# Optimization experiments

Measured on AMD Instinct MI355X. Metric: run time of the kernel, lower is better.

Reference implementation:

```python
import jax, jax.numpy as jnp
import numpy as np

EPS = 1e-8
CG_TOL = 1e-4
S_SIGMA = 8   # bilateral grid spatial downsampling
N_BINS = 9    # bilateral grid range bins (intensity in [0,1])


def _conv2d(x, k):
    # x [C,H,W], k [kh,kw] -> same-padded cross-correlation, per channel
    kh, kw = k.shape
    out = jax.lax.conv_general_dilated(x[:, None], k[None, None], (1, 1),
                                       [(kh // 2, kh // 2), (kw // 2, kw // 2)])
    return out[:, 0]


def _conv2d_T(x, k):
    return _conv2d(x, k[::-1, ::-1])


def _conv_bank(x, ks):
    # x [C,H,W], ks [N,kh,kw] -> [N,C,H,W]
    n, kh, kw = ks.shape
    out = jax.lax.conv_general_dilated(x[:, None], ks[:, None], (1, 1),
                                       [(kh // 2, kh // 2), (kw // 2, kw // 2)])
    return out.transpose(1, 0, 2, 3)


def _conv_bank_T(v, ks):
    # v [N,C,H,W] -> sum_n conv(v[n], flip(ks[n])) : [C,H,W]
    n, kh, kw = ks.shape
    lhs = v.transpose(1, 0, 2, 3)          # [C,N,H,W]
    rhs = ks[:, ::-1, ::-1][None]          # [1,N,kh,kw]
    out = jax.lax.conv_general_dilated(lhs, rhs, (1, 1),
                                       [(kh // 2, kh // 2), (kw // 2, kw // 2)])
    return out[:, 0]


def _deconv_grad(blurred, x, kernel, dkw, dks, rkw, rks, rpow, reg_targets):
    # gradient of E(x) = sum_i dkw_i ||dk_i * (k*x - b)||^2
    #                  + sum_j rkw_j sum |rk_j*x - t_j|^{p_j}
    Kx = _conv2d(x, kernel) - blurred
    d = _conv_bank(Kx, dks)                                    # [Nd,C,H,W]
    g = _conv2d_T(_conv_bank_T(2.0 * dkw[:, None, None, None] * d, dks), kernel)
    v = _conv_bank(x, rks) - reg_targets                       # [Nr,C,H,W]
    av = jnp.abs(v) + EPS
    phi = jnp.sign(v) * av ** (rpow[:, None, None, None] - 1.0)
    g = g + _conv_bank_T(rkw[:, None, None, None] * rpow[:, None, None, None] * phi, rks)
    return g


def _deconv_alpha(blurred, x, kernel, dkw, dks, rkw, rks, rpow, reg_targets, p):
    # exact line search for the quadratic part, Gauss-Newton for |.|^p prior
    g = _deconv_grad(blurred, x, kernel, dkw, dks, rkw, rks, rpow, reg_targets)
    num = -jnp.sum(g * p)
    Kp = _conv2d(p, kernel)
    dKp = _conv_bank(Kp, dks)
    den = jnp.sum(2.0 * dkw[:, None, None, None] * dKp ** 2)
    v = _conv_bank(x, rks) - reg_targets
    Rp = _conv_bank(p, rks)
    w = (rkw * rpow * (rpow - 1.0))[:, None, None, None]
    den = den + jnp.sum(w * (jnp.abs(v) + EPS) ** (rpow[:, None, None, None] - 2.0) * Rp ** 2)
    return num / (den + 1e-12)


def _deconv_prior(x, rks, thr):
    # soft-shrinkage of filtered responses -> regularization targets
    v = _conv_bank(x, rks)
    return jnp.sign(v) * jnp.maximum(jnp.abs(v) - thr[:, None, None, None], 0.0)


def _conv_axis(g, f, axis):
    k = f.shape[0]; r = k // 2; L = g.shape[axis]
    pad = [(0, 0)] * g.ndim; pad[axis] = (r, r)
    gp = jnp.pad(g, pad)
    out = jnp.zeros_like(g)
    for t in range(k):  # fixed small tap count
        out = out + f[t] * jax.lax.slice_in_dim(gp, t, t + L, axis=axis)
    return out


def _bilateral_channel(I, fs, fr):
    # learned-filter bilateral grid: splat -> separable filter (fs,fs,fr) -> trilinear slice
    H, W = I.shape
    gh, gw = H // S_SIGMA, W // S_SIGMA
    Ic = jnp.clip(I, 0.0, 1.0)
    yy, xx = jnp.meshgrid(jnp.arange(H), jnp.arange(W), indexing="ij")
    yi = yy // S_SIGMA; xi = xx // S_SIGMA
    zi = jnp.clip(jnp.round(Ic * (N_BINS - 1)).astype(jnp.int32), 0, N_BINS - 1)
    flat = ((yi * gw + xi) * N_BINS + zi).ravel()
    gv = jnp.zeros(gh * gw * N_BINS, Ic.dtype).at[flat].add(Ic.ravel())
    gw_ = jnp.zeros(gh * gw * N_BINS, Ic.dtype).at[flat].add(1.0)
    g2 = jnp.stack([gv, gw_], -1).reshape(gh, gw, N_BINS, 2)
    g2 = _conv_axis(_conv_axis(_conv_axis(g2, fs, 0), fs, 1), fr, 2)
    yf = yy / S_SIGMA; xf = xx / S_SIGMA; zf = Ic * (N_BINS - 1)

    def corners(f, n):
        c0 = jnp.clip(jnp.floor(f).astype(jnp.int32), 0, n - 1)
        c1 = jnp.minimum(c0 + 1, n - 1)
        w = jnp.clip(f - c0, 0.0, 1.0)
        return c0, c1, w

    y0, y1, wy = corners(yf, gh)
    x0, x1, wx = corners(xf, gw)
    z0, z1, wz = corners(zf, N_BINS)
    acc = jnp.zeros(I.shape + (2,), Ic.dtype)
    for yc, wyc in ((y0, 1 - wy), (y1, wy)):
        for xc, wxc in ((x0, 1 - wx), (x1, wx)):
            for zc, wzc in ((z0, 1 - wz), (z1, wz)):
                acc = acc + (wyc * wxc * wzc)[..., None] * g2[yc, xc, zc]
    return acc[..., 0] / (acc[..., 1] + 1e-8)


def _forward(blurred_batch, kernel_batch, data_kernels, data_kernel_weights,
             reg_kernels, reg_kernel_weights, reg_powers, filter_s, filter_r,
             reg_thresholds, num_cg_iter):
    num_stages = filter_s.shape[0]
    n_reg = reg_kernels.shape[1]

    def single(blurred, kernel):
        def cg(x, idx, reg_targets):
            dkw = data_kernel_weights[idx]; dks = data_kernels[idx]
            rkw = reg_kernel_weights[idx]; rks = reg_kernels[idx]; rp = reg_powers[idx]
            g = _deconv_grad(blurred, x, kernel, dkw, dks, rkw, rks, rp, reg_targets)
            r = -g
            r_norm = jnp.sum(r * r)
            r0 = r_norm

            def body(i, carry):
                x, r, p, rn, done = carry
                alpha = _deconv_alpha(blurred, x, kernel, dkw, dks, rkw, rks, rp, reg_targets, p)
                x1 = x + alpha * p
                g1 = _deconv_grad(blurred, x1, kernel, dkw, dks, rkw, rks, rp, reg_targets)
                r1 = -g1
                nrn = jnp.sum(r1 * r1)
                beta = nrn / (rn + 1e-20)
                conv_now = nrn < CG_TOL * r0
                p1 = r1 + beta * p
                x_n = jnp.where(done, x, x1)
                r_n = jnp.where(done, r, r1)
                rn_n = jnp.where(done, rn, nrn)
                p_n = jnp.where(done | conv_now, p, p1)
                return (x_n, r_n, p_n, rn_n, done | conv_now)

            carry = (x, r, r, r_norm, jnp.array(False))
            x, _, _, _, _ = jax.lax.fori_loop(0, num_cg_iter, body, carry)
            return x

        x = cg(blurred, 0, jnp.zeros((n_reg,) + blurred.shape, blurred.dtype))
        for stage in range(num_stages):
            x = jax.vmap(lambda ch: _bilateral_channel(ch, filter_s[stage], filter_r[stage]))(x)
            reg_targets = _deconv_prior(x, reg_kernels[stage + 1], reg_thresholds[stage])
            x = cg(x, stage + 1, reg_targets)
        return x

    return jax.vmap(single)(blurred_batch, kernel_batch)


def setup_inputs() -> dict:
    key = jax.random.key(0)
    k1, k2 = jax.random.split(key)
    B, C, H, W, KS = 2, 3, 512, 512, 15
    blurred = jax.random.uniform(k1, (B, C, H, W), jnp.float32)
    kern = jax.random.uniform(k2, (B, KS, KS), jnp.float32)
    kern = kern / jnp.sum(kern, axis=(1, 2), keepdims=True)  # normalized PSFs

    ns = 1; c = 2  # num_stages, kernel center (5x5)
    rk = np.zeros((ns + 1, 5, 5, 5), np.float32)
    rk[:, 0, c, c] = -1.0; rk[:, 0, c + 1, c] = 1.0
    rk[:, 1, c, c] = -1.0; rk[:, 1, c, c + 1] = 1.0
    rk[:, 2, c, c] = 1.0; rk[:, 2, c + 1, c] = -1.0
    rk[:, 2, c, c + 1] = -1.0; rk[:, 2, c + 1, c + 1] = 1.0
    rk[:, 3, c - 1, c] = 1.0; rk[:, 3, c, c] = -2.0; rk[:, 3, c + 1, c] = 1.0
    rk[:, 4, c, c - 1] = 1.0; rk[:, 4, c, c] = -2.0; rk[:, 4, c, c + 1] = 1.0
    dk = np.zeros((ns + 1, 6, 5, 5), np.float32)
    dk[:, 0, c, c] = 1.0
    dk[:, 1:] = rk
    dkw = np.zeros((ns + 1, 6), np.float32); dkw[:, 0] = 1.0
    rkw = np.zeros((ns + 1, 5), np.float32)
    rkw[0, :] = 0.001; rkw[1:, :] = 0.05
    rpow = np.full((ns + 1, 5), 2.0, np.float32)
    fs = np.zeros((ns, 11), np.float32); fs[:, 3:8] = [0.0, 1.0, 2.0, 1.0, 0.0]
    fr = np.tile(np.array([0.0, 1.0, 2.0, 1.0, 0.0], np.float32), (ns, 1))
    thr = np.tile(np.array([0.065, 0.065, 0.0325, 0.0325, 0.0325], np.float32), (ns, 1))

    return {
        "blurred_batch": blurred,
        "kernel_batch": kern,
        "data_kernels": jnp.asarray(dk),
        "data_kernel_weights": jnp.asarray(dkw),
        "reg_kernels": jnp.asarray(rk),
        "reg_kernel_weights": jnp.asarray(rkw),
        "reg_powers": jnp.asarray(rpow),
        "filter_s": jnp.asarray(fs),
        "filter_r": jnp.asarray(fr),
        "reg_thresholds": jnp.asarray(thr),
        "num_cg_iter": 5,
    }


def reference(blurred_batch, kernel_batch, data_kernels, data_kernel_weights,
              reg_kernels, reg_kernel_weights, reg_powers, filter_s, filter_r,
              reg_thresholds, num_cg_iter):
    return _forward(blurred_batch, kernel_batch, data_kernels, data_kernel_weights,
                    reg_kernels, reg_kernel_weights, reg_powers, filter_s, filter_r,
                    reg_thresholds, num_cg_iter)
```

## Files before the change

### kernel.cpp

```cpp
#include <hip/hip_runtime.h>

constexpr int Bn = 2, Cn = 3, Hh = 512, Ww = 512;
constexpr int KS = 15, KR = 7;
constexpr int NDK = 6, NRK = 5;
constexpr int GH = 64, GW = 64, NBn = 9, SS = 8;
constexpr float EPSf = 1e-8f;
constexpr float CGTOL = 1e-4f;
constexpr int PLANE = Hh * Ww;
constexpr int CHW = Cn * PLANE;
constexpr int BX = 64, BY = 16;
constexpr int GXc = Ww / BX, GYc = Hh / BY;
constexpr int PB = GXc * GYc * Cn;
constexpr int SA = 80, THt = 30;
constexpr int S2W = 72, S2H = 24;
constexpr int PHW = 68, PHH = 20;
constexpr int PHG = (PHW / 4) * PHH;
constexpr int NITER = 5;

struct CgState { float alpha, beta, rn, r0; int done, pflag; int pad0, pad1; };

struct SolveInfo {
    int fastBank;
    int allrp2;
    int nd;
    int pad;
    float sctot;
    float dsc[NDK];
    int ddy[NDK], ddx[NDK];
    float C[81];
};

__device__ __forceinline__ float blockReduce(float v, float* red, int tid) {
    red[tid] = v; __syncthreads();
    for (int s = 128; s > 0; s >>= 1) { if (tid < s) red[tid] += red[tid + s]; __syncthreads(); }
    float r = red[0]; __syncthreads();
    return r;
}

__global__ __launch_bounds__(128)
void k_comp(const float* __restrict__ dkw, const float* __restrict__ dks,
            const float* __restrict__ rkw, const float* __restrict__ rpw,
            const float* __restrict__ rks, SolveInfo* si)
{
    const int idx = blockIdx.x;
    SolveInfo* s = si + idx;
    const float* dkw_i = dkw + idx * NDK;
    const float* dks_i = dks + (size_t)idx * NDK * 25;
    const float* rkw_i = rkw + idx * NRK;
    const float* rpw_i = rpw + idx * NRK;
    const float* rks_i = rks + (size_t)idx * NRK * 25;
    const int t = threadIdx.x;
    if (t < 81) {
        int oy = t / 9 - 4, ox = t % 9 - 4;
        float acc = 0.f;
        for (int m = 0; m < NRK; m++) {
            float wm = rkw_i[m], rp = rpw_i[m];
            float ch = wm * rp * (rp - 1.f);
            if (ch == 0.f) continue;
            for (int ay = 0; ay < 5; ay++)
                for (int ax = 0; ax < 5; ax++) {
                    int by = ay - oy, bx = ax - ox;
                    if (by < 0 || by >= 5 || bx < 0 || bx >= 5) continue;
                    acc += ch * rks_i[m * 25 + ay * 5 + ax] * rks_i[m * 25 + by * 5 + bx];
                }
        }
        s->C[t] = acc;
    }
    if (t == 81) {
        int fast = 1, nd = 0; float tot = 0.f;
        for (int n = 0; n < NDK; n++) {
            if (dkw_i[n] == 0.f) continue;
            int cnt = 0, pos = -1;
            for (int q = 0; q < 25; q++) if (dks_i[n * 25 + q] != 0.f) { cnt++; pos = q; }
            if (cnt > 1) fast = 0;
            if (cnt == 1 && nd < NDK) {
                float v = dks_i[n * 25 + pos];
                s->dsc[nd] = 2.f * dkw_i[n] * v * v;
                s->ddy[nd] = pos / 5 - 2; s->ddx[nd] = pos % 5 - 2;
                tot += s->dsc[nd]; nd++;
            }
        }
        s->fastBank = fast; s->nd = fast ? nd : 0; s->sctot = tot;
    }
    if (t == 82) {
        int ok = 1;
        for (int m = 0; m < NRK; m++) {
            float wm = rkw_i[m], rp = rpw_i[m];
            if (wm != 0.f && rp != 2.f && wm * rp * (rp - 1.f) != 0.f) ok = 0;
        }
        s->allrp2 = ok;
    }
}

__global__ __launch_bounds__(256)
void k_conv15(const float* __restrict__ src, const float* __restrict__ rb,
              const float* __restrict__ pbuf, float* __restrict__ aux2,
              const float* __restrict__ sub, float* __restrict__ out,
              const float* __restrict__ kernB, float* __restrict__ part,
              const SolveInfo* __restrict__ si,
              const CgState* __restrict__ st, const int* __restrict__ ncg,
              int iter, int mode)
{
    const int pz = blockIdx.z, b = pz / Cn, c = pz % Cn;
    const CgState s = st[b];
    if (mode == 2 && (s.done != 0 || iter >= *ncg)) return;
    __shared__ __align__(16) float tile[SA * THt];
    __shared__ float red[256];
    const int tx = threadIdx.x, ty = threadIdx.y, tid = ty * 16 + tx;
    const int ox0 = blockIdx.x * BX, oy0 = blockIdx.y * BY;
    const int baseP = pz * PLANE;
    const float beta = s.beta; const int pf = s.pflag;
    const float* kp = kernB + b * 225;

    float nm = 0.f;
    for (int i = tid; i < 78 * THt; i += 256) {
        int ly = i / 78, lx = i % 78;
        int gy = oy0 - KR + ly, gx = ox0 - KR + lx;
        float v = 0.f;
        if (gy >= 0 && gy < Hh && gx >= 0 && gx < Ww) {
            int gi = baseP + gy * Ww + gx;
            if (mode == 2) {
                float rv = rb[gi], pv = pbuf[gi];
                v = pf ? fmaf(beta, pv, rv) : pv;
                if (ly >= KR && ly < KR + BY && lx >= KR && lx < KR + BX) {
                    nm = fmaf(rv, v, nm);
                    aux2[gi] = v;
                }
            } else {
                v = src[gi];
                if (mode == 0 && ly >= KR && ly < KR + BY && lx >= KR && lx < KR + BX)
                    aux2[gi] = v;
            }
        }
        tile[ly * SA + lx] = v;
    }
    __syncthreads();

    const int colbase = tx * 4;
    float a0 = 0.f, a1 = 0.f, a2 = 0.f, a3 = 0.f;
    for (int i = 0; i < KS; i++) {
        const float4* rp4 = reinterpret_cast<const float4*>(&tile[(ty + i) * SA + colbase]);
        float f[20];
        #pragma unroll
        for (int s5 = 0; s5 < 5; s5++) {
            float4 w4 = rp4[s5];
            f[s5 * 4] = w4.x; f[s5 * 4 + 1] = w4.y; f[s5 * 4 + 2] = w4.z; f[s5 * 4 + 3] = w4.w;
        }
        const float* kr = kp + i * 15;
        #pragma unroll
        for (int j = 0; j < KS; j++) {
            float kv = kr[j];
            a0 = fmaf(kv, f[j], a0); a1 = fmaf(kv, f[j + 1], a1);
            a2 = fmaf(kv, f[j + 2], a2); a3 = fmaf(kv, f[j + 3], a3);
        }
    }
    const int gi = baseP + (oy0 + ty) * Ww + ox0 + colbase;
    if (sub) {
        float4 sv = *reinterpret_cast<const float4*>(&sub[gi]);
        a0 -= sv.x; a1 -= sv.y; a2 -= sv.z; a3 -= sv.w;
    }
    if (si->fastBank) {
        const int gy = oy0 + ty, gx0 = ox0 + colbase;
        if (gy >= 2 && gy <= Hh - 3 && gx0 >= 2 && gx0 + 3 <= Ww - 3) {
            float sc = si->sctot;
            a0 *= sc; a1 *= sc; a2 *= sc; a3 *= sc;
        } else {
            float m0 = 0.f, m1 = 0.f, m2 = 0.f, m3 = 0.f;
            int ndl = si->nd;
            for (int n = 0; n < ndl; n++) {
                float sc = si->dsc[n]; int dy = si->ddy[n], dx = si->ddx[n];
                if (gy - dy < 0 || gy - dy >= Hh) continue;
                if (gx0     - dx >= 0 && gx0     - dx < Ww) m0 += sc;
                if (gx0 + 1 - dx >= 0 && gx0 + 1 - dx < Ww) m1 += sc;
                if (gx0 + 2 - dx >= 0 && gx0 + 2 - dx < Ww) m2 += sc;
                if (gx0 + 3 - dx >= 0 && gx0 + 3 - dx < Ww) m3 += sc;
            }
            a0 *= m0; a1 *= m1; a2 *= m2; a3 *= m3;
        }
    }
    *reinterpret_cast<float4*>(&out[gi]) = make_float4(a0, a1, a2, a3);
    if (mode == 2) {
        float tot = blockReduce(nm, red, tid);
        if (tid == 0) {
            int blk = c * (GXc * GYc) + blockIdx.y * GXc + blockIdx.x;
            part[((size_t)b * 4 + 0) * PB + blk] = tot;
        }
    }
}

__global__ __launch_bounds__(256)
void k_bank(const float* __restrict__ sbuf, float* __restrict__ tbuf,
            const float* __restrict__ dks, const float* __restrict__ dkw,
            const SolveInfo* __restrict__ si,
            const CgState* __restrict__ st, const int* __restrict__ ncg,
            int iter, int mode)
{
    if (si->fastBank) return;
    const int pz = blockIdx.z, b = pz / Cn;
    if (mode == 1 && (st[b].done != 0 || iter >= *ncg)) return;
    __shared__ __align__(16) float sl[S2W * S2H];
    __shared__ __align__(16) float dl[PHW * PHH];
    __shared__ float dkk[NDK * 25];
    __shared__ float dww[NDK];
    const int tx = threadIdx.x, ty = threadIdx.y, tid = ty * 16 + tx;
    const int ox0 = blockIdx.x * BX, oy0 = blockIdx.y * BY;
    const int baseP = pz * PLANE;
    const int colbase = tx * 4;
    for (int i = tid; i < NDK * 25; i += 256) dkk[i] = dks[i];
    if (tid < NDK) dww[tid] = dkw[tid];
    for (int i = tid; i < S2W * S2H; i += 256) {
        int ly = i / S2W, lx = i % S2W;
        int gy = oy0 - 4 + ly, gx = ox0 - 4 + lx;
        sl[i] = (gy >= 0 && gy < Hh && gx >= 0 && gx < Ww) ? sbuf[baseP + gy * Ww + gx] : 0.f;
    }
    __syncthreads();
    float t0 = 0.f, t1 = 0.f, t2 = 0.f, t3 = 0.f;
    for (int n = 0; n < NDK; n++) {
        float wn = 2.f * dww[n];
        if (wn == 0.f) continue;
        float dnr[25];
        #pragma unroll
        for (int q = 0; q < 25; q++) dnr[q] = dkk[n * 25 + q];
        for (int t = tid; t < PHG; t += 256) {
            int zy = t / 17, zx0 = (t % 17) * 4;
            int gy = oy0 - 2 + zy, gx0 = ox0 - 2 + zx0;
            float v0 = 0.f, v1 = 0.f, v2 = 0.f, v3 = 0.f;
            #pragma unroll
            for (int a = 0; a < 5; a++) {
                bool rz = dnr[a*5]==0.f && dnr[a*5+1]==0.f && dnr[a*5+2]==0.f &&
                          dnr[a*5+3]==0.f && dnr[a*5+4]==0.f;
                if (rz) continue;
                const float4* s4 = reinterpret_cast<const float4*>(&sl[(zy + a) * S2W + zx0]);
                float4 u0 = s4[0], u1 = s4[1];
                float f8[8] = {u0.x,u0.y,u0.z,u0.w,u1.x,u1.y,u1.z,u1.w};
                #pragma unroll
                for (int bb = 0; bb < 5; bb++) {
                    float kv = dnr[a * 5 + bb];
                    if (kv != 0.f) {
                        v0 = fmaf(kv, f8[bb], v0); v1 = fmaf(kv, f8[bb+1], v1);
                        v2 = fmaf(kv, f8[bb+2], v2); v3 = fmaf(kv, f8[bb+3], v3);
                    }
                }
            }
            bool gyin = (gy >= 0 && gy < Hh);
            if (!gyin || gx0     < 0 || gx0     >= Ww) v0 = 0.f;
            if (!gyin || gx0 + 1 < 0 || gx0 + 1 >= Ww) v1 = 0.f;
            if (!gyin || gx0 + 2 < 0 || gx0 + 2 >= Ww) v2 = 0.f;
            if (!gyin || gx0 + 3 < 0 || gx0 + 3 >= Ww) v3 = 0.f;
            *reinterpret_cast<float4*>(&dl[zy * PHW + zx0]) = make_float4(v0, v1, v2, v3);
        }
        __syncthreads();
        float c0 = 0.f, c1 = 0.f, c2 = 0.f, c3 = 0.f;
        #pragma unroll
        for (int a = 0; a < 5; a++) {
            int fr = 4 - a;
            bool rz = dnr[fr*5]==0.f && dnr[fr*5+1]==0.f && dnr[fr*5+2]==0.f &&
                      dnr[fr*5+3]==0.f && dnr[fr*5+4]==0.f;
            if (rz) continue;
            const float4* q4 = reinterpret_cast<const float4*>(&dl[(ty + a) * PHW + colbase]);
            float4 u0 = q4[0], u1 = q4[1];
            float f8[8] = {u0.x,u0.y,u0.z,u0.w,u1.x,u1.y,u1.z,u1.w};
            #pragma unroll
            for (int bb = 0; bb < 5; bb++) {
                float kv = dnr[fr * 5 + (4 - bb)];
                if (kv != 0.f) {
                    c0 = fmaf(kv, f8[bb], c0); c1 = fmaf(kv, f8[bb+1], c1);
                    c2 = fmaf(kv, f8[bb+2], c2); c3 = fmaf(kv, f8[bb+3], c3);
                }
            }
        }
        t0 = fmaf(wn, c0, t0); t1 = fmaf(wn, c1, t1);
        t2 = fmaf(wn, c2, t2); t3 = fmaf(wn, c3, t3);
        __syncthreads();
    }
    const int gi = baseP + (oy0 + ty) * Ww + ox0 + colbase;
    *reinterpret_cast<float4*>(&tbuf[gi]) = make_float4(t0, t1, t2, t3);
}

__global__ __launch_bounds__(256)
void k_hess(const float* __restrict__ kx, const float* __restrict__ wb,
            const float* __restrict__ pn,
            float* __restrict__ qb, const float* __restrict__ kernB,
            const float* __restrict__ rks, const float* __restrict__ rkw,
            const float* __restrict__ rpw, const SolveInfo* __restrict__ si,
            float* __restrict__ part, const CgState* __restrict__ st,
            const int* __restrict__ ncg, int iter)
{
    if (!si->allrp2) return;
    const int pz = blockIdx.z, b = pz / Cn, c = pz % Cn;
    const CgState s = st[b];
    if (s.done != 0 || iter >= *ncg) return;
    __shared__ __align__(16) float wt[SA * THt];
    __shared__ __align__(16) float s2[S2W * S2H];
    __shared__ __align__(16) float sC[81];
    __shared__ float rk5[NRK * 25];
    __shared__ float srkw[NRK], srpw[NRK];
    __shared__ float red[256];
    float* ph = wt;
    const int tx = threadIdx.x, ty = threadIdx.y, tid = ty * 16 + tx;
    const int ox0 = blockIdx.x * BX, oy0 = blockIdx.y * BY;
    const int baseP = pz * PLANE;
    const float* wsrc = si->fastBank ? kx : wb;
    const float* kp = kernB + b * 225;

    for (int i = tid; i < 81; i += 256) sC[i] = si->C[i];
    for (int i = tid; i < NRK * 25; i += 256) rk5[i] = rks[i];
    if (tid < NRK) { srkw[tid] = rkw[tid]; srpw[tid] = rpw[tid]; }

    for (int i = tid; i < 78 * THt; i += 256) {
        int ly = i / 78, lx = i % 78;
        int gy = oy0 - KR + ly, gx = ox0 - KR + lx;
        wt[ly * SA + lx] = (gy >= 0 && gy < Hh && gx >= 0 && gx < Ww)
                           ? wsrc[baseP + gy * Ww + gx] : 0.f;
    }
    for (int i = tid; i < S2W * S2H; i += 256) {
        int ly = i / S2W, lx = i % S2W;
        int gy = oy0 - 4 + ly, gx = ox0 - 4 + lx;
        s2[i] = (gy >= 0 && gy < Hh && gx >= 0 && gx < Ww)
                ? pn[baseP + gy * Ww + gx] : 0.f;
    }
    __syncthreads();

    const int colbase = tx * 4;
    float a0 = 0.f, a1 = 0.f, a2 = 0.f, a3 = 0.f;
    for (int i = 0; i < KS; i++) {
        const float4* rp4 = reinterpret_cast<const float4*>(&wt[(ty + i) * SA + colbase]);
        float f[20];
        #pragma unroll
        for (int s5 = 0; s5 < 5; s5++) {
            float4 w4 = rp4[s5];
            f[s5 * 4] = w4.x; f[s5 * 4 + 1] = w4.y; f[s5 * 4 + 2] = w4.z; f[s5 * 4 + 3] = w4.w;
        }
        const float* kr = kp + (14 - i) * 15;
        #pragma unroll
        for (int j = 0; j < KS; j++) {
            float kv = kr[14 - j];
            a0 = fmaf(kv, f[j], a0); a1 = fmaf(kv, f[j + 1], a1);
            a2 = fmaf(kv, f[j + 2], a2); a3 = fmaf(kv, f[j + 3], a3);
        }
    }

    const bool blkInterior = (oy0 >= 2) && (oy0 + BY - 1 <= Hh - 3) &&
                             (ox0 >= 2) && (ox0 + BX - 1 <= Ww - 3);
    if (blkInterior) {
        #pragma unroll
        for (int oy = 0; oy < 9; oy++) {
            float cr[9]; bool nz = false;
            #pragma unroll
            for (int ox = 0; ox < 9; ox++) { cr[ox] = sC[oy * 9 + ox]; nz = nz || (cr[ox] != 0.f); }
            if (!nz) continue;
            const float4* s4 = reinterpret_cast<const float4*>(&s2[(ty + oy) * S2W + colbase]);
            float4 u0 = s4[0], u1 = s4[1], u2 = s4[2];
            float f12[12] = {u0.x,u0.y,u0.z,u0.w,u1.x,u1.y,u1.z,u1.w,u2.x,u2.y,u2.z,u2.w};
            #pragma unroll
            for (int ox = 0; ox < 9; ox++) {
                float kv = cr[ox];
                if (kv != 0.f) {
                    a0 = fmaf(kv, f12[ox], a0); a1 = fmaf(kv, f12[ox + 1], a1);
                    a2 = fmaf(kv, f12[ox + 2], a2); a3 = fmaf(kv, f12[ox + 3], a3);
                }
            }
        }
    } else {
        __syncthreads();
        for (int m = 0; m < NRK; m++) {
            float wm = srkw[m], rp = srpw[m];
            float coefH = wm * rp * (rp - 1.f);
            if (coefH == 0.f) continue;
            float rmr[25];
            #pragma unroll
            for (int q = 0; q < 25; q++) rmr[q] = rk5[m * 25 + q];
            for (int t = tid; t < PHG; t += 256) {
                int zy = t / 17, zx0 = (t % 17) * 4;
                int gy = oy0 - 2 + zy, gx0 = ox0 - 2 + zx0;
                float v0 = 0.f, v1 = 0.f, v2 = 0.f, v3 = 0.f;
                #pragma unroll
                for (int a = 0; a < 5; a++) {
                    bool rz = rmr[a*5]==0.f && rmr[a*5+1]==0.f && rmr[a*5+2]==0.f &&
                              rmr[a*5+3]==0.f && rmr[a*5+4]==0.f;
                    if (rz) continue;
                    const float4* s4 = reinterpret_cast<const float4*>(&s2[(zy + a) * S2W + zx0]);
                    float4 u0 = s4[0], u1 = s4[1];
                    float f8[8] = {u0.x,u0.y,u0.z,u0.w,u1.x,u1.y,u1.z,u1.w};
                    #pragma unroll
                    for (int bb = 0; bb < 5; bb++) {
                        float kv = rmr[a * 5 + bb];
                        if (kv != 0.f) {
                            v0 = fmaf(kv, f8[bb], v0); v1 = fmaf(kv, f8[bb+1], v1);
                            v2 = fmaf(kv, f8[bb+2], v2); v3 = fmaf(kv, f8[bb+3], v3);
                        }
                    }
                }
                bool gyin = (gy >= 0 && gy < Hh);
                if (!gyin || gx0     < 0 || gx0     >= Ww) v0 = 0.f;
                if (!gyin || gx0 + 1 < 0 || gx0 + 1 >= Ww) v1 = 0.f;
                if (!gyin || gx0 + 2 < 0 || gx0 + 2 >= Ww) v2 = 0.f;
                if (!gyin || gx0 + 3 < 0 || gx0 + 3 >= Ww) v3 = 0.f;
                *reinterpret_cast<float4*>(&ph[zy * PHW + zx0]) =
                    make_float4(coefH * v0, coefH * v1, coefH * v2, coefH * v3);
            }
            __syncthreads();
            #pragma unroll
            for (int a = 0; a < 5; a++) {
                int fr = 4 - a;
                bool rz = rmr[fr*5]==0.f && rmr[fr*5+1]==0.f && rmr[fr*5+2]==0.f &&
                          rmr[fr*5+3]==0.f && rmr[fr*5+4]==0.f;
                if (rz) continue;
                const float4* q4 = reinterpret_cast<const float4*>(&ph[(ty + a) * PHW + colbase]);
                float4 u0 = q4[0], u1 = q4[1];
                float f8[8] = {u0.x,u0.y,u0.z,u0.w,u1.x,u1.y,u1.z,u1.w};
                #pragma unroll
                for (int bb = 0; bb < 5; bb++) {
                    float kv = rmr[fr * 5 + (4 - bb)];
                    if (kv != 0.f) {
                        a0 = fmaf(kv, f8[bb], a0); a1 = fmaf(kv, f8[bb+1], a1);
                        a2 = fmaf(kv, f8[bb+2], a2); a3 = fmaf(kv, f8[bb+3], a3);
                    }
                }
            }
            __syncthreads();
        }
    }

    const int gy = oy0 + ty, gx0 = ox0 + colbase;
    const int gi = baseP + gy * Ww + gx0;
    *reinterpret_cast<float4*>(&qb[gi]) = make_float4(a0, a1, a2, a3);
    int li = (ty + 4) * S2W + colbase + 4;
    float redv = s2[li] * a0 + s2[li + 1] * a1 + s2[li + 2] * a2 + s2[li + 3] * a3;
    float tot = blockReduce(redv, red, tid);
    if (tid == 0) {
        int blk = c * (GXc * GYc) + blockIdx.y * GXc + blockIdx.x;
        part[((size_t)b * 4 + 1) * PB + blk] = tot;
    }
}

__global__ __launch_bounds__(256)
void k_gradL(const float* __restrict__ kx, const float* __restrict__ wb,
             const float* __restrict__ xg,
             const float* __restrict__ rb, const float* __restrict__ pbuf,
             const float* __restrict__ tgt, const float* __restrict__ thr,
             float* __restrict__ outb,
             float* __restrict__ pout, const float* __restrict__ kernB,
             const float* __restrict__ rks, const float* __restrict__ rkw,
             const float* __restrict__ rpw, const SolveInfo* __restrict__ si,
             float* __restrict__ part, const CgState* __restrict__ st,
             const int* __restrict__ ncg, int iter, int mode)
{
    if (mode == 1 && si->allrp2) return;
    const int pz = blockIdx.z, b = pz / Cn, c = pz % Cn;
    const CgState s = st[b];
    if (mode == 1 && (s.done != 0 || iter >= *ncg)) return;
    __shared__ __align__(16) float wt[SA * THt];
    __shared__ __align__(16) float s2[S2W * S2H];
    __shared__ __align__(16) float sC[81];
    __shared__ float rk5[NRK * 25];
    __shared__ float srkw[NRK], srpw[NRK], sthr[NRK];
    __shared__ float red[256];
    float* ph = wt;
    const int tx = threadIdx.x, ty = threadIdx.y, tid = ty * 16 + tx;
    const int ox0 = blockIdx.x * BX, oy0 = blockIdx.y * BY;
    const int baseP = pz * PLANE;
    const float beta = s.beta; const int pf = s.pflag;
    const float* wsrc = si->fastBank ? kx : wb;
    const float* kp = kernB + b * 225;

    for (int i = tid; i < 81; i += 256) sC[i] = si->C[i];
    for (int i = tid; i < NRK * 25; i += 256) rk5[i] = rks[i];
    if (tid < NRK) {
        srkw[tid] = rkw[tid]; srpw[tid] = rpw[tid];
        sthr[tid] = thr ? thr[tid] : 0.f;
    }

    for (int i = tid; i < 78 * THt; i += 256) {
        int ly = i / 78, lx = i % 78;
        int gy = oy0 - KR + ly, gx = ox0 - KR + lx;
        wt[ly * SA + lx] = (gy >= 0 && gy < Hh && gx >= 0 && gx < Ww)
                           ? wsrc[baseP + gy * Ww + gx] : 0.f;
    }
    for (int i = tid; i < S2W * S2H; i += 256) {
        int ly = i / S2W, lx = i % S2W;
        int gy = oy0 - 4 + ly, gx = ox0 - 4 + lx;
        float v = 0.f;
        if (gy >= 0 && gy < Hh && gx >= 0 && gx < Ww) {
            int gi = baseP + gy * Ww + gx;
            if (mode == 0) v = xg[gi];
            else { float rv = rb[gi], pv = pbuf[gi]; v = pf ? fmaf(beta, pv, rv) : pv; }
        }
        s2[i] = v;
    }
    __syncthreads();

    const int colbase = tx * 4;
    float a0 = 0.f, a1 = 0.f, a2 = 0.f, a3 = 0.f;
    for (int i = 0; i < KS; i++) {
        const float4* rp4 = reinterpret_cast<const float4*>(&wt[(ty + i) * SA + colbase]);
        float f[20];
        #pragma unroll
        for (int s5 = 0; s5 < 5; s5++) {
            float4 w4 = rp4[s5];
            f[s5 * 4] = w4.x; f[s5 * 4 + 1] = w4.y; f[s5 * 4 + 2] = w4.z; f[s5 * 4 + 3] = w4.w;
        }
        const float* kr = kp + (14 - i) * 15;
        #pragma unroll
        for (int j = 0; j < KS; j++) {
            float kv = kr[14 - j];
            a0 = fmaf(kv, f[j], a0); a1 = fmaf(kv, f[j + 1], a1);
            a2 = fmaf(kv, f[j + 2], a2); a3 = fmaf(kv, f[j + 3], a3);
        }
    }

    const bool blkInterior = (oy0 >= 2) && (oy0 + BY - 1 <= Hh - 3) &&
                             (ox0 >= 2) && (ox0 + BX - 1 <= Ww - 3);
    if (mode == 0 && si->allrp2 && thr == nullptr && blkInterior) {
        #pragma unroll
        for (int oy = 0; oy < 9; oy++) {
            float cr[9]; bool nz = false;
            #pragma unroll
            for (int ox = 0; ox < 9; ox++) { cr[ox] = sC[oy * 9 + ox]; nz = nz || (cr[ox] != 0.f); }
            if (!nz) continue;
            const float4* s4 = reinterpret_cast<const float4*>(&s2[(ty + oy) * S2W + colbase]);
            float4 u0 = s4[0], u1 = s4[1], u2 = s4[2];
            float f12[12] = {u0.x,u0.y,u0.z,u0.w,u1.x,u1.y,u1.z,u1.w,u2.x,u2.y,u2.z,u2.w};
            #pragma unroll
            for (int ox = 0; ox < 9; ox++) {
                float kv = cr[ox];
                if (kv != 0.f) {
                    a0 = fmaf(kv, f12[ox], a0); a1 = fmaf(kv, f12[ox + 1], a1);
                    a2 = fmaf(kv, f12[ox + 2], a2); a3 = fmaf(kv, f12[ox + 3], a3);
                }
            }
        }
    } else {
        __syncthreads();
        for (int m = 0; m < NRK; m++) {
            float wm = srkw[m], rp = srpw[m];
            if (wm == 0.f) continue;
            float rmr[25];
            #pragma unroll
            for (int q = 0; q < 25; q++) rmr[q] = rk5[m * 25 + q];
            const float* tgm = (mode == 1 && tgt)
                ? tgt + ((size_t)(b * NRK + m)) * CHW + (size_t)c * PLANE : nullptr;
            const float coefG = wm * rp;
            const float coefH = wm * rp * (rp - 1.f);
            const float thrm = sthr[m];

            for (int t = tid; t < PHG; t += 256) {
                int zy = t / 17, zx0 = (t % 17) * 4;
                int gy = oy0 - 2 + zy, gx0 = ox0 - 2 + zx0;
                float v0 = 0.f, v1 = 0.f, v2 = 0.f, v3 = 0.f;
                #pragma unroll
                for (int a = 0; a < 5; a++) {
                    bool rz = rmr[a*5]==0.f && rmr[a*5+1]==0.f && rmr[a*5+2]==0.f &&
                              rmr[a*5+3]==0.f && rmr[a*5+4]==0.f;
                    if (rz) continue;
                    const float4* s4 = reinterpret_cast<const float4*>(&s2[(zy + a) * S2W + zx0]);
                    float4 u0 = s4[0], u1 = s4[1];
                    float f8[8] = {u0.x,u0.y,u0.z,u0.w,u1.x,u1.y,u1.z,u1.w};
                    #pragma unroll
                    for (int bb = 0; bb < 5; bb++) {
                        float kv = rmr[a * 5 + bb];
                        if (kv != 0.f) {
                            v0 = fmaf(kv, f8[bb], v0); v1 = fmaf(kv, f8[bb+1], v1);
                            v2 = fmaf(kv, f8[bb+2], v2); v3 = fmaf(kv, f8[bb+3], v3);
                        }
                    }
                }
                bool gyin = (gy >= 0 && gy < Hh);
                float o0 = 0.f, o1 = 0.f, o2 = 0.f, o3 = 0.f;
                #pragma unroll
                for (int j = 0; j < 4; j++) {
                    int gx = gx0 + j;
                    if (!gyin || gx < 0 || gx >= Ww) continue;
                    float v = (j == 0) ? v0 : (j == 1) ? v1 : (j == 2) ? v2 : v3;
                    float o;
                    if (mode == 0) {
                        if (thr) {
                            float sgv = (v > 0.f) ? 1.f : ((v < 0.f) ? -1.f : 0.f);
                            v = sgv * fminf(fabsf(v), thrm);
                        }
                        float sg = (v > 0.f) ? 1.f : ((v < 0.f) ? -1.f : 0.f);
                        float av = fabsf(v) + EPSf;
                        o = coefG * sg * ((rp == 2.f) ? av : powf(av, rp - 1.f));
                    } else {
                        float fac = 1.f;
                        if (rp != 2.f) {
                            float vx = 0.f;
                            for (int a = 0; a < 5; a++)
                                for (int bb = 0; bb < 5; bb++) {
                                    int yy = gy - 2 + a, xx = gx - 2 + bb;
                                    if (yy >= 0 && yy < Hh && xx >= 0 && xx < Ww)
                                        vx = fmaf(rmr[a * 5 + bb], xg[baseP + yy * Ww + xx], vx);
                                }
                            if (tgm) vx -= tgm[gy * Ww + gx];
                            fac = powf(fabsf(vx) + EPSf, rp - 2.f);
                        }
                        o = coefH * fac * v;
                    }
                    if (j == 0) o0 = o; else if (j == 1) o1 = o; else if (j == 2) o2 = o; else o3 = o;
                }
                *reinterpret_cast<float4*>(&ph[zy * PHW + zx0]) = make_float4(o0, o1, o2, o3);
            }
            __syncthreads();
            #pragma unroll
            for (int a = 0; a < 5; a++) {
                int fr = 4 - a;
                bool rz = rmr[fr*5]==0.f && rmr[fr*5+1]==0.f && rmr[fr*5+2]==0.f &&
                          rmr[fr*5+3]==0.f && rmr[fr*5+4]==0.f;
                if (rz) continue;
                const float4* q4 = reinterpret_cast<const float4*>(&ph[(ty + a) * PHW + colbase]);
                float4 u0 = q4[0], u1 = q4[1];
                float f8[8] = {u0.x,u0.y,u0.z,u0.w,u1.x,u1.y,u1.z,u1.w};
                #pragma unroll
                for (int bb = 0; bb < 5; bb++) {
                    float kv = rmr[fr * 5 + (4 - bb)];
                    if (kv != 0.f) {
                        a0 = fmaf(kv, f8[bb], a0); a1 = fmaf(kv, f8[bb+1], a1);
                        a2 = fmaf(kv, f8[bb+2], a2); a3 = fmaf(kv, f8[bb+3], a3);
                    }
                }
            }
            __syncthreads();
        }
    }

    const int gi = baseP + (oy0 + ty) * Ww + ox0 + colbase;
    float redv;
    if (mode == 0) {
        float r0v = -a0, r1v = -a1, r2v = -a2, r3v = -a3;
        float4 rv4 = make_float4(r0v, r1v, r2v, r3v);
        *reinterpret_cast<float4*>(&outb[gi]) = rv4;
        *reinterpret_cast<float4*>(&pout[gi]) = rv4;
        redv = r0v * r0v + r1v * r1v + r2v * r2v + r3v * r3v;
    } else {
        *reinterpret_cast<float4*>(&outb[gi]) = make_float4(a0, a1, a2, a3);
        int li = (ty + 4) * S2W + colbase + 4;
        redv = s2[li] * a0 + s2[li + 1] * a1 + s2[li + 2] * a2 + s2[li + 3] * a3;
    }
    float tot = blockReduce(redv, red, tid);
    if (tid == 0) {
        int blk = c * (GXc * GYc) + blockIdx.y * GXc + blockIdx.x;
        int slot = (mode == 0) ? 2 : 1;
        part[((size_t)b * 4 + slot) * PB + blk] = tot;
    }
}

__global__ __launch_bounds__(256)
void k_axpy(float4* __restrict__ x, float4* __restrict__ r,
            const float4* __restrict__ pn,
            const float4* __restrict__ q, float* __restrict__ part,
            const CgState* __restrict__ st, const int* __restrict__ ncg, int iter)
{
    const int b = blockIdx.y;
    const CgState s = st[b];
    if (s.done != 0 || iter >= *ncg) return;
    __shared__ float red[256];
    const int tid = threadIdx.x;
    const int idx = b * (CHW / 4) + blockIdx.x * 256 + tid;
    float4 pc = pn[idx], rv = r[idx], qv = q[idx], xv = x[idx];
    xv.x = fmaf(s.alpha, pc.x, xv.x); xv.y = fmaf(s.alpha, pc.y, xv.y);
    xv.z = fmaf(s.alpha, pc.z, xv.z); xv.w = fmaf(s.alpha, pc.w, xv.w);
    rv.x = fmaf(-s.alpha, qv.x, rv.x); rv.y = fmaf(-s.alpha, qv.y, rv.y);
    rv.z = fmaf(-s.alpha, qv.z, rv.z); rv.w = fmaf(-s.alpha, qv.w, rv.w);
    x[idx] = xv; r[idx] = rv;
    float nr = rv.x * rv.x + rv.y * rv.y + rv.z * rv.z + rv.w * rv.w;
    float tot = blockReduce(nr, red, tid);
    if (tid == 0) part[((size_t)b * 4 + 2) * PB + blockIdx.x] = tot;
}

__global__ __launch_bounds__(256)
void k_fin_alpha(const float* __restrict__ part, CgState* st,
                 const int* __restrict__ ncg, int iter)
{
    const int b = blockIdx.x, tid = threadIdx.x;
    __shared__ float red[256];
    if (st[b].done != 0 || iter >= *ncg) { if (tid == 0) st[b].alpha = 0.f; return; }
    float sn = 0.f, sd = 0.f;
    for (int i = tid; i < PB; i += 256) {
        sn += part[((size_t)b * 4 + 0) * PB + i];
        sd += part[((size_t)b * 4 + 1) * PB + i];
    }
    float num = blockReduce(sn, red, tid);
    float den = blockReduce(sd, red, tid);
    if (tid == 0) st[b].alpha = num / (den + 1e-12f);
}

__global__ __launch_bounds__(256)
void k_fin_iter(const float* __restrict__ part, CgState* st,
                const int* __restrict__ ncg, int iter, int mode)
{
    const int b = blockIdx.x, tid = threadIdx.x;
    __shared__ float red[256];
    if (mode == 1 && (st[b].done != 0 || iter >= *ncg)) { if (tid == 0) st[b].pflag = 0; return; }
    float s = 0.f;
    for (int i = tid; i < PB; i += 256) s += part[((size_t)b * 4 + 2) * PB + i];
    float nrn = blockReduce(s, red, tid);
    if (tid == 0) {
        if (mode == 0) {
            st[b].rn = nrn; st[b].r0 = nrn; st[b].done = 0; st[b].pflag = 0;
            st[b].beta = 0.f; st[b].alpha = 0.f;
        } else {
            float beta = nrn / (st[b].rn + 1e-20f);
            int conv = (nrn < CGTOL * st[b].r0) ? 1 : 0;
            st[b].beta = beta; st[b].rn = nrn;
            st[b].pflag = conv ? 0 : 1;
            if (conv) st[b].done = 1;
        }
    }
}

__global__ __launch_bounds__(64)
void k_splat(const float* __restrict__ x, float* __restrict__ grid)
{
    __shared__ float bins[NBn * 2];
    const int tid = threadIdx.y * 8 + threadIdx.x;
    if (tid < NBn * 2) bins[tid] = 0.f;
    __syncthreads();
    const int pz = blockIdx.z;
    const int gy = blockIdx.y, gx = blockIdx.x;
    const int py = gy * 8 + threadIdx.y, px = gx * 8 + threadIdx.x;
    float I = x[(size_t)pz * PLANE + py * Ww + px];
    float Ic = fminf(fmaxf(I, 0.f), 1.f);
    int zi = (int)rintf(Ic * (NBn - 1));
    zi = min(max(zi, 0), NBn - 1);
    atomicAdd(&bins[zi * 2], Ic);
    atomicAdd(&bins[zi * 2 + 1], 1.f);
    __syncthreads();
    if (tid < NBn * 2)
        grid[(size_t)pz * GH * GW * NBn * 2 + ((size_t)gy * GW + gx) * NBn * 2 + tid] = bins[tid];
}

__global__ __launch_bounds__(256)
void k_blur(const float* __restrict__ in, float* __restrict__ out,
            const float* __restrict__ taps, int ntaps, int axis)
{
    const int id = blockIdx.x * 256 + threadIdx.x;
    const int total = Bn * Cn * GH * GW * NBn;
    if (id >= total) return;
    const int z = id % NBn;
    const int x = (id / NBn) % GW;
    const int y = (id / (NBn * GW)) % GH;
    const int p = id / (NBn * GW * GH);
    int coord, lim; long stride;
    if (axis == 0)      { coord = y; lim = GH;  stride = (long)GW * NBn * 2; }
    else if (axis == 1) { coord = x; lim = GW;  stride = NBn * 2; }
    else                { coord = z; lim = NBn; stride = 2; }
    const long base = (((long)(p * GH + y) * GW + x) * NBn + z) * 2;
    const int r = ntaps / 2;
    float a0 = 0.f, a1 = 0.f;
    for (int t = 0; t < ntaps; t++) {
        int cc = coord + t - r;
        if (cc < 0 || cc >= lim) continue;
        float w = taps[t];
        long ofs = base + (long)(cc - coord) * stride;
        a0 = fmaf(w, in[ofs], a0);
        a1 = fmaf(w, in[ofs + 1], a1);
    }
    out[base] = a0; out[base + 1] = a1;
}

__global__ __launch_bounds__(256)
void k_slice(const float* __restrict__ xin, const float* __restrict__ grid,
             float* __restrict__ xout)
{
    const int pz = blockIdx.z;
    const int id = blockIdx.x * 256 + threadIdx.x;
    const int py = id / Ww, px = id % Ww;
    float I = xin[(size_t)pz * PLANE + id];
    float Ic = fminf(fmaxf(I, 0.f), 1.f);
    float yf = (float)py / SS, xf = (float)px / SS, zf = Ic * (NBn - 1);
    int y0 = min(max((int)floorf(yf), 0), GH - 1); int y1 = min(y0 + 1, GH - 1);
    float wy = fminf(fmaxf(yf - (float)y0, 0.f), 1.f);
    int x0 = min(max((int)floorf(xf), 0), GW - 1); int x1 = min(x0 + 1, GW - 1);
    float wx = fminf(fmaxf(xf - (float)x0, 0.f), 1.f);
    int z0 = min(max((int)floorf(zf), 0), NBn - 1); int z1 = min(z0 + 1, NBn - 1);
    float wz = fminf(fmaxf(zf - (float)z0, 0.f), 1.f);
    const float* gp = grid + (size_t)pz * GH * GW * NBn * 2;
    const int   ys[2] = { y0, y1 };  const float wys[2] = { 1.f - wy, wy };
    const int   xs[2] = { x0, x1 };  const float wxs[2] = { 1.f - wx, wx };
    const int   zs[2] = { z0, z1 };  const float wzs[2] = { 1.f - wz, wz };
    float a0 = 0.f, a1 = 0.f;
    for (int iy = 0; iy < 2; iy++)
        for (int ix = 0; ix < 2; ix++)
            for (int iz = 0; iz < 2; iz++) {
                float w = wys[iy] * wxs[ix] * wzs[iz];
                size_t idx = (((size_t)ys[iy] * GW + xs[ix]) * NBn + zs[iz]) * 2;
                a0 = fmaf(w, gp[idx], a0);
                a1 = fmaf(w, gp[idx + 1], a1);
            }
    xout[(size_t)pz * PLANE + id] = a0 / (a1 + 1e-8f);
}

__global__ __launch_bounds__(256)
void k_prior(const float* __restrict__ x, float* __restrict__ tgt,
             const float* __restrict__ rks, const float* __restrict__ thr,
             const SolveInfo* __restrict__ si)
{
    if (si->allrp2) return;
    const int pz = blockIdx.z, b = pz / Cn, c = pz % Cn;
    __shared__ float xl[24 * 24];
    __shared__ float rkk[NRK * 25];
    __shared__ float sthr[NRK];
    const int tx = threadIdx.x, ty = threadIdx.y, tid = ty * 16 + tx;
    const int ox0 = blockIdx.x * 16, oy0 = blockIdx.y * 16;
    const int baseP = pz * PLANE;
    for (int i = tid; i < NRK * 25; i += 256) rkk[i] = rks[i];
    if (tid < NRK) sthr[tid] = thr[tid];
    for (int i = tid; i < 24 * 24; i += 256) {
        int ly = i / 24, lx = i % 24;
        int gy = oy0 - 2 + ly, gx = ox0 - 2 + lx;
        xl[i] = (gy >= 0 && gy < Hh && gx >= 0 && gx < Ww) ? x[baseP + gy * Ww + gx] : 0.f;
    }
    __syncthreads();
    const int pix = (oy0 + ty) * Ww + (ox0 + tx);
    for (int m = 0; m < NRK; m++) {
        const float* rm = &rkk[m * 25];
        float v = 0.f;
        #pragma unroll
        for (int a = 0; a < 5; a++)
            #pragma unroll
            for (int bb = 0; bb < 5; bb++)
                v = fmaf(rm[a * 5 + bb], xl[(ty + a) * 24 + (tx + bb)], v);
        float sg = (v > 0.f) ? 1.f : ((v < 0.f) ? -1.f : 0.f);
        tgt[((size_t)(b * NRK + m)) * CHW + (size_t)c * PLANE + pix] =
            sg * fmaxf(fabsf(v) - sthr[m], 0.f);
    }
}

extern "C" void kernel_launch(void* const* d_in, const int* in_sizes, int n_in,
                              void* d_out, int out_size, void* d_ws, size_t ws_size,
                              hipStream_t stream)
{
    const float* blurred = (const float*)d_in[0];
    const float* kern    = (const float*)d_in[1];
    const float* dks     = (const float*)d_in[2];
    const float* dkw     = (const float*)d_in[3];
    const float* rks     = (const float*)d_in[4];
    const float* rkw     = (const float*)d_in[5];
    const float* rpw     = (const float*)d_in[6];
    const float* fs      = (const float*)d_in[7];
    const float* fr      = (const float*)d_in[8];
    const float* thr     = (const float*)d_in[9];
    const int*   ncg     = (const int*)d_in[10];
    (void)in_sizes; (void)n_in; (void)out_size; (void)ws_size;

    float* w = (float*)d_ws;
    size_t off = 0;
    auto alloc = [&](size_t n) { float* p = w + off; off += n; return p; };
    float* xb    = alloc((size_t)Bn * CHW);
    float* pbufA = alloc((size_t)Bn * CHW);
    float* pbufB = alloc((size_t)Bn * CHW);
    float* rbuf  = alloc((size_t)Bn * CHW);
    float* kx    = alloc((size_t)Bn * CHW);
    float* wb    = alloc((size_t)Bn * CHW);
    float* qb    = alloc((size_t)Bn * CHW);
    float* tg    = alloc((size_t)Bn * NRK * CHW);
    float* g0    = alloc((size_t)Bn * Cn * GH * GW * NBn * 2);
    float* g1    = alloc((size_t)Bn * Cn * GH * GW * NBn * 2);
    float* part  = alloc((size_t)Bn * 4 * PB);
    CgState* st = (CgState*)(w + off); off += Bn * 8;
    SolveInfo* sinf = (SolveInfo*)(w + off); off += 2 * ((sizeof(SolveInfo) + 3) / 4);

    dim3 tb(16, 16), grd(GXc, GYc, Bn * Cn);

    k_comp<<<2, 128, 0, stream>>>(dkw, dks, rkw, rpw, rks, sinf);

    auto solve = [&](int idx, const float* tgt, const float* thr_i, int initmode) {
        const float* dks_i = dks + (size_t)idx * NDK * 25;
        const float* dkw_i = dkw + (size_t)idx * NDK;
        const float* rks_i = rks + (size_t)idx * NRK * 25;
        const float* rkw_i = rkw + (size_t)idx * NRK;
        const float* rpw_i = rpw + (size_t)idx * NRK;
        const SolveInfo* si = sinf + idx;
        k_conv15<<<grd, tb, 0, stream>>>(initmode == 0 ? blurred : xb, nullptr, nullptr,
                                         initmode == 0 ? xb : nullptr, blurred, kx, kern,
                                         nullptr, si, st, ncg, 0, initmode == 0 ? 0 : 3);
        k_bank<<<grd, tb, 0, stream>>>(kx, wb, dks_i, dkw_i, si, st, ncg, 0, 0);
        k_gradL<<<grd, tb, 0, stream>>>(kx, wb, xb, nullptr, nullptr, tgt, thr_i,
                                        rbuf, pbufA, kern,
                                        rks_i, rkw_i, rpw_i, si, part, st, ncg, 0, 0);
        k_fin_iter<<<Bn, 256, 0, stream>>>(part, st, ncg, 0, 0);
        float* pcur = pbufA;
        float* pnxt = pbufB;
        for (int i = 0; i < NITER; i++) {
            k_conv15<<<grd, tb, 0, stream>>>(nullptr, rbuf, pcur, pnxt, nullptr, kx, kern,
                                             part, si, st, ncg, i, 2);
            k_bank<<<grd, tb, 0, stream>>>(kx, wb, dks_i, dkw_i, si, st, ncg, i, 1);
            k_hess<<<grd, tb, 0, stream>>>(kx, wb, pnxt, qb, kern,
                                           rks_i, rkw_i, rpw_i, si, part, st, ncg, i);
            k_gradL<<<grd, tb, 0, stream>>>(kx, wb, xb, rbuf, pnxt, tgt, thr_i, qb, nullptr, kern,
                                            rks_i, rkw_i, rpw_i, si, part, st, ncg, i, 1);
            k_fin_alpha<<<Bn, 256, 0, stream>>>(part, st, ncg, i);
            k_axpy<<<dim3(PB, Bn), 256, 0, stream>>>((float4*)xb, (float4*)rbuf,
                                                     (const float4*)pnxt,
                                                     (const float4*)qb, part, st, ncg, i);
            k_fin_iter<<<Bn, 256, 0, stream>>>(part, st, ncg, i, 1);
            float* tswap = pcur; pcur = pnxt; pnxt = tswap;
        }
    };

    solve(0, nullptr, nullptr, 0);

    dim3 sb(8, 8), sg(GW, GH, Bn * Cn);
    k_splat<<<sg, sb, 0, stream>>>(xb, g0);
    const int totalg = Bn * Cn * GH * GW * NBn;
    k_blur<<<(totalg + 255) / 256, 256, 0, stream>>>(g0, g1, fs, 11, 0);
    k_blur<<<(totalg + 255) / 256, 256, 0, stream>>>(g1, g0, fs, 11, 1);
    k_blur<<<(totalg + 255) / 256, 256, 0, stream>>>(g0, g1, fr, 5, 2);
    k_slice<<<dim3(PLANE / 256, 1, Bn * Cn), 256, 0, stream>>>(xb, g1, xb);

    k_prior<<<dim3(Ww / 16, Hh / 16, Bn * Cn), tb, 0, stream>>>(xb, tg, rks + NRK * 25, thr,
                                                                sinf + 1);

    solve(1, tg, thr, 1);

    hipMemcpyAsync(d_out, xb, (size_t)Bn * CHW * sizeof(float),
                   hipMemcpyDeviceToDevice, stream);
}
```

Measured before the change: 1.337 ms.

## Fold CG alpha and residual-norm reductions into axpy kernel

Each axpy block now recomputes alpha from the partial sums itself, so the separate k_fin_alpha launch is gone. A last-block-done atomic counter lets the final axpy block do the residual-norm reduction and the beta/convergence update, so k_fin_iter is also dropped inside the loop. This removes two small serial launches per CG iteration. In exchange every block redundantly reads the PB partials, and correctness now relies on atomics and threadfences.

```diff
diff --git a/kernel.cpp b/kernel.cpp
--- a/kernel.cpp
+++ b/kernel.cpp
@@ -37,10 +37,25 @@
     return r;
 }
 
+__device__ __forceinline__ bool lastBlockDone(unsigned int* c, unsigned int nb,
+                                              int tid, int* sflag) {
+    __syncthreads();
+    if (tid == 0) {
+        __threadfence();
+        unsigned int old = atomicAdd(c, 1u);
+        *sflag = (old == nb - 1u) ? 1 : 0;
+    }
+    __syncthreads();
+    bool last = (*sflag != 0);
+    if (last && tid == 0) __threadfence();
+    if (last) __syncthreads();
+    return last;
+}
+
 __global__ __launch_bounds__(128)
 void k_comp(const float* __restrict__ dkw, const float* __restrict__ dks,
             const float* __restrict__ rkw, const float* __restrict__ rpw,
-            const float* __restrict__ rks, SolveInfo* si)
+            const float* __restrict__ rks, SolveInfo* si, unsigned int* cnt)
 {
     const int idx = blockIdx.x;
     SolveInfo* s = si + idx;
@@ -50,6 +65,7 @@
     const float* rpw_i = rpw + idx * NRK;
     const float* rks_i = rks + (size_t)idx * NRK * 25;
     const int t = threadIdx.x;
+    if (idx == 0 && t < 8) cnt[t] = 0u;
     if (t < 81) {
         int oy = t / 9 - 4, ox = t % 9 - 4;
         float acc = 0.f;
@@ -70,10 +86,10 @@
         int fast = 1, nd = 0; float tot = 0.f;
         for (int n = 0; n < NDK; n++) {
             if (dkw_i[n] == 0.f) continue;
-            int cnt = 0, pos = -1;
-            for (int q = 0; q < 25; q++) if (dks_i[n * 25 + q] != 0.f) { cnt++; pos = q; }
-            if (cnt > 1) fast = 0;
-            if (cnt == 1 && nd < NDK) {
+            int cntz = 0, pos = -1;
+            for (int q = 0; q < 25; q++) if (dks_i[n * 25 + q] != 0.f) { cntz++; pos = q; }
+            if (cntz > 1) fast = 0;
+            if (cntz == 1 && nd < NDK) {
                 float v = dks_i[n * 25 + pos];
                 s->dsc[nd] = 2.f * dkw_i[n] * v * v;
                 s->ddy[nd] = pos / 5 - 2; s->ddx[nd] = pos % 5 - 2;
@@ -646,42 +662,47 @@
 
 __global__ __launch_bounds__(256)
 void k_axpy(float4* __restrict__ x, float4* __restrict__ r,
-            const float4* __restrict__ pn,
-            const float4* __restrict__ q, float* __restrict__ part,
-            const CgState* __restrict__ st, const int* __restrict__ ncg, int iter)
+            const float4* __restrict__ pn, const float4* __restrict__ q,
+            float* __restrict__ part, CgState* st,
+            const int* __restrict__ ncg, int iter, unsigned int* cnt)
 {
     const int b = blockIdx.y;
     const CgState s = st[b];
     if (s.done != 0 || iter >= *ncg) return;
     __shared__ float red[256];
+    __shared__ int sflag;
     const int tid = threadIdx.x;
+    float sn = 0.f, sd = 0.f;
+    for (int i = tid; i < PB; i += 256) {
+        sn += part[((size_t)b * 4 + 0) * PB + i];
+        sd += part[((size_t)b * 4 + 1) * PB + i];
+    }
+    float num = blockReduce(sn, red, tid);
+    float den = blockReduce(sd, red, tid);
+    const float alpha = num / (den + 1e-12f);
     const int idx = b * (CHW / 4) + blockIdx.x * 256 + tid;
     float4 pc = pn[idx], rv = r[idx], qv = q[idx], xv = x[idx];
-    xv.x = fmaf(s.alpha, pc.x, xv.x); xv.y = fmaf(s.alpha, pc.y, xv.y);
-    xv.z = fmaf(s.alpha, pc.z, xv.z); xv.w = fmaf(s.alpha, pc.w, xv.w);
-    rv.x = fmaf(-s.alpha, qv.x, rv.x); rv.y = fmaf(-s.alpha, qv.y, rv.y);
-    rv.z = fmaf(-s.alpha, qv.z, rv.z); rv.w = fmaf(-s.alpha, qv.w, rv.w);
+    xv.x = fmaf(alpha, pc.x, xv.x); xv.y = fmaf(alpha, pc.y, xv.y);
+    xv.z = fmaf(alpha, pc.z, xv.z); xv.w = fmaf(alpha, pc.w, xv.w);
+    rv.x = fmaf(-alpha, qv.x, rv.x); rv.y = fmaf(-alpha, qv.y, rv.y);
+    rv.z = fmaf(-alpha, qv.z, rv.z); rv.w = fmaf(-alpha, qv.w, rv.w);
     x[idx] = xv; r[idx] = rv;
     float nr = rv.x * rv.x + rv.y * rv.y + rv.z * rv.z + rv.w * rv.w;
     float tot = blockReduce(nr, red, tid);
     if (tid == 0) part[((size_t)b * 4 + 2) * PB + blockIdx.x] = tot;
-}
-
-__global__ __launch_bounds__(256)
-void k_fin_alpha(const float* __restrict__ part, CgState* st,
-                 const int* __restrict__ ncg, int iter)
-{
-    const int b = blockIdx.x, tid = threadIdx.x;
-    __shared__ float red[256];
-    if (st[b].done != 0 || iter >= *ncg) { if (tid == 0) st[b].alpha = 0.f; return; }
-    float sn = 0.f, sd = 0.f;
-    for (int i = tid; i < PB; i += 256) {
-        sn += part[((size_t)b * 4 + 0) * PB + i];
-        sd += part[((size_t)b * 4 + 1) * PB + i];
-    }
-    float num = blockReduce(sn, red, tid);
-    float den = blockReduce(sd, red, tid);
-    if (tid == 0) st[b].alpha = num / (den + 1e-12f);
+    if (lastBlockDone(&cnt[2 + b], PB, tid, &sflag)) {
+        float s2 = 0.f;
+        for (int i = tid; i < PB; i += 256) s2 += part[((size_t)b * 4 + 2) * PB + i];
+        float nrn = blockReduce(s2, red, tid);
+        if (tid == 0) {
+            float beta = nrn / (st[b].rn + 1e-20f);
+            int conv = (nrn < CGTOL * st[b].r0) ? 1 : 0;
+            st[b].beta = beta; st[b].rn = nrn;
+            st[b].pflag = conv ? 0 : 1;
+            if (conv) st[b].done = 1;
+            cnt[2 + b] = 0u;
+        }
+    }
 }
 
 __global__ __launch_bounds__(256)
@@ -859,12 +880,13 @@
     float* part  = alloc((size_t)Bn * 4 * PB);
     CgState* st = (CgState*)(w + off); off += Bn * 8;
     SolveInfo* sinf = (SolveInfo*)(w + off); off += 2 * ((sizeof(SolveInfo) + 3) / 4);
+    unsigned int* cnt = (unsigned int*)(w + off); off += 8;
 
     dim3 tb(16, 16), grd(GXc, GYc, Bn * Cn);
 
-    k_comp<<<2, 128, 0, stream>>>(dkw, dks, rkw, rpw, rks, sinf);
-
-    auto solve = [&](int idx, const float* tgt, const float* thr_i, int initmode) {
+    k_comp<<<2, 128, 0, stream>>>(dkw, dks, rkw, rpw, rks, sinf, cnt);
+
+    auto solve = [&](int idx, const float* tgt_i, const float* thr_i, int initmode) {
         const float* dks_i = dks + (size_t)idx * NDK * 25;
         const float* dkw_i = dkw + (size_t)idx * NDK;
         const float* rks_i = rks + (size_t)idx * NRK * 25;
@@ -875,7 +897,7 @@
                                          initmode == 0 ? xb : nullptr, blurred, kx, kern,
                                          nullptr, si, st, ncg, 0, initmode == 0 ? 0 : 3);
         k_bank<<<grd, tb, 0, stream>>>(kx, wb, dks_i, dkw_i, si, st, ncg, 0, 0);
-        k_gradL<<<grd, tb, 0, stream>>>(kx, wb, xb, nullptr, nullptr, tgt, thr_i,
+        k_gradL<<<grd, tb, 0, stream>>>(kx, wb, xb, nullptr, nullptr, tgt_i, thr_i,
                                         rbuf, pbufA, kern,
                                         rks_i, rkw_i, rpw_i, si, part, st, ncg, 0, 0);
         k_fin_iter<<<Bn, 256, 0, stream>>>(part, st, ncg, 0, 0);
@@ -887,13 +909,11 @@
             k_bank<<<grd, tb, 0, stream>>>(kx, wb, dks_i, dkw_i, si, st, ncg, i, 1);
             k_hess<<<grd, tb, 0, stream>>>(kx, wb, pnxt, qb, kern,
                                            rks_i, rkw_i, rpw_i, si, part, st, ncg, i);
-            k_gradL<<<grd, tb, 0, stream>>>(kx, wb, xb, rbuf, pnxt, tgt, thr_i, qb, nullptr, kern,
-                                            rks_i, rkw_i, rpw_i, si, part, st, ncg, i, 1);
-            k_fin_alpha<<<Bn, 256, 0, stream>>>(part, st, ncg, i);
+            k_gradL<<<grd, tb, 0, stream>>>(kx, wb, xb, rbuf, pnxt, tgt_i, thr_i, qb, nullptr,
+                                            kern, rks_i, rkw_i, rpw_i, si, part, st, ncg, i, 1);
             k_axpy<<<dim3(PB, Bn), 256, 0, stream>>>((float4*)xb, (float4*)rbuf,
-                                                     (const float4*)pnxt,
-                                                     (const float4*)qb, part, st, ncg, i);
-            k_fin_iter<<<Bn, 256, 0, stream>>>(part, st, ncg, i, 1);
+                                                     (const float4*)pnxt, (const float4*)qb,
+                                                     part, st, ncg, i, cnt);
             float* tswap = pcur; pcur = pnxt; pnxt = tswap;
         }
     };
```

After: 1.774 ms. 1.33x slower.
